# Performance work log

Hardware: AMD Instinct MI355X
Metric: run time of the kernel (lower is better)

The kernel has to match this reference:

```python
import jax, jax.numpy as jnp
import numpy as np

N_NODES = 10000
N_EDGES = 200000
CHANNELS = 128
# lm -> l map for spherical harmonics up to l=3 (1+3+5+7 = 16 components)
L_OF_LM = jnp.array([0, 1, 1, 1, 2, 2, 2, 2, 2, 3, 3, 3, 3, 3, 3, 3], dtype=jnp.int32)


def setup_inputs() -> dict:
    key = jax.random.key(0)
    k1, k2, k3, k4, k5 = jax.random.split(key, 5)
    node_feats = jax.random.normal(k1, (N_NODES, CHANNELS), dtype=jnp.float32)
    edge_attrs = jax.random.normal(k2, (N_EDGES, 16), dtype=jnp.float32)
    tp_weights = jax.random.normal(k3, (N_EDGES, 4, CHANNELS), dtype=jnp.float32)
    sender_list = jax.random.randint(k4, (N_EDGES,), 0, N_NODES, dtype=jnp.int64)
    receiver_list = jnp.sort(jax.random.randint(k5, (N_EDGES,), 0, N_NODES, dtype=jnp.int64))
    return {
        "node_feats": node_feats,
        "edge_attrs": edge_attrs,
        "tp_weights": tp_weights,
        "sender_list": sender_list,
        "receiver_list": receiver_list,
    }


def reference(node_feats, edge_attrs, tp_weights, sender_list, receiver_list):
    # Gather sender features: [E, C]
    sender_feats = node_feats[sender_list]
    # Broadcast per-l weights to the 16 lm components: [E, 16, C]
    w_lm = tp_weights[:, L_OF_LM, :]
    # Per-edge invariant tensor product message: [E, 16, C]
    messages = sender_feats[:, None, :] * edge_attrs[:, :, None] * w_lm
    # Scatter-add to receivers: [N, 16, C]
    out = jax.ops.segment_sum(messages, receiver_list, num_segments=N_NODES)
    return out
```

## Files before the change

### kernel.cpp

```cpp
#include <hip/hip_runtime.h>


#define N_NODES  10000
#define N_EDGES  200000
#define CHANNELS 128

__global__ __launch_bounds__(128) void imp_tp_kernel(
    const float* __restrict__ node_feats,
    const float* __restrict__ edge_attrs,
    const float* __restrict__ tp_weights,
    const int*   __restrict__ sender_list,
    const int*   __restrict__ receiver_list,
    float* __restrict__ out)
{
    const int n = blockIdx.x;
    const int c = threadIdx.x;

    int lo = 0, hi = N_EDGES;
    while (lo < hi) { int mid = (lo + hi) >> 1; if (receiver_list[mid] < n)     lo = mid + 1; else hi = mid; }
    const int seg_start = lo;
    hi = N_EDGES;
    while (lo < hi) { int mid = (lo + hi) >> 1; if (receiver_list[mid] < n + 1) lo = mid + 1; else hi = mid; }
    const int seg_end = lo;

    float acc[16];
    #pragma unroll
    for (int i = 0; i < 16; ++i) acc[i] = 0.0f;

    const float4* __restrict__ ea4 = (const float4*)edge_attrs;

    for (int e = seg_start; e < seg_end; ++e) {
        const int s = sender_list[e];
        const float sf = node_feats[(size_t)s * CHANNELS + c];

        const float* __restrict__ w = tp_weights + (size_t)e * 4 * CHANNELS + c;
        const float w0 = w[0 * CHANNELS];
        const float w1 = w[1 * CHANNELS];
        const float w2 = w[2 * CHANNELS];
        const float w3 = w[3 * CHANNELS];

        const float4 a0 = ea4[(size_t)e * 4 + 0];
        const float4 a1 = ea4[(size_t)e * 4 + 1];
        const float4 a2 = ea4[(size_t)e * 4 + 2];
        const float4 a3 = ea4[(size_t)e * 4 + 3];

        const float p0 = sf * w0;
        const float p1 = sf * w1;
        const float p2 = sf * w2;
        const float p3 = sf * w3;

        acc[0]  = fmaf(p0, a0.x, acc[0]);
        acc[1]  = fmaf(p1, a0.y, acc[1]);
        acc[2]  = fmaf(p1, a0.z, acc[2]);
        acc[3]  = fmaf(p1, a0.w, acc[3]);
        acc[4]  = fmaf(p2, a1.x, acc[4]);
        acc[5]  = fmaf(p2, a1.y, acc[5]);
        acc[6]  = fmaf(p2, a1.z, acc[6]);
        acc[7]  = fmaf(p2, a1.w, acc[7]);
        acc[8]  = fmaf(p2, a2.x, acc[8]);
        acc[9]  = fmaf(p3, a2.y, acc[9]);
        acc[10] = fmaf(p3, a2.z, acc[10]);
        acc[11] = fmaf(p3, a2.w, acc[11]);
        acc[12] = fmaf(p3, a3.x, acc[12]);
        acc[13] = fmaf(p3, a3.y, acc[13]);
        acc[14] = fmaf(p3, a3.z, acc[14]);
        acc[15] = fmaf(p3, a3.w, acc[15]);
    }

    float* __restrict__ o = out + (size_t)n * 16 * CHANNELS + c;
    #pragma unroll
    for (int lm = 0; lm < 16; ++lm) o[lm * CHANNELS] = acc[lm];
}

extern "C" void kernel_launch(void* const* d_in, const int* in_sizes, int n_in,
                              void* d_out, int out_size, void* d_ws, size_t ws_size,
                              hipStream_t stream) {
    const float* node_feats    = (const float*)d_in[0];
    const float* edge_attrs    = (const float*)d_in[1];
    const float* tp_weights    = (const float*)d_in[2];
    const int*   sender_list   = (const int*)d_in[3];
    const int*   receiver_list = (const int*)d_in[4];
    float* out = (float*)d_out;

    imp_tp_kernel<<<N_NODES, CHANNELS, 0, stream>>>(
        node_feats, edge_attrs, tp_weights, sender_list, receiver_list, out);
}
```

Measured before the change: 589.0 us.

## Precompute CSR row pointers and process one node per wavefront with float2 channels

```diff
diff --git a/kernel.cpp b/kernel.cpp
--- a/kernel.cpp
+++ b/kernel.cpp
@@ -3,73 +3,92 @@
 
 #define N_NODES  10000
 #define N_EDGES  200000
-#define CHANNELS 128
 
-__global__ __launch_bounds__(128) void imp_tp_kernel(
+__global__ __launch_bounds__(256) void bounds_kernel(
+    const int* __restrict__ recv, int* __restrict__ row_ptr)
+{
+    const int i = blockIdx.x * 256 + threadIdx.x;
+    if (i > N_NODES) return;
+    int lo = 0, hi = N_EDGES;
+    while (lo < hi) { int mid = (lo + hi) >> 1; if (recv[mid] < i) lo = mid + 1; else hi = mid; }
+    row_ptr[i] = lo;
+}
+
+struct Edge {
+    float2 sf, w0, w1, w2, w3;
+    float4 a0, a1, a2, a3;
+};
+
+#define FMA2(ac, p, s) do { (ac).x = fmaf((p).x, (s), (ac).x); (ac).y = fmaf((p).y, (s), (ac).y); } while (0)
+
+__global__ __launch_bounds__(256) void imp_tp_kernel(
     const float* __restrict__ node_feats,
     const float* __restrict__ edge_attrs,
     const float* __restrict__ tp_weights,
     const int*   __restrict__ sender_list,
-    const int*   __restrict__ receiver_list,
+    const int*   __restrict__ row_ptr,
     float* __restrict__ out)
 {
-    const int n = blockIdx.x;
-    const int c = threadIdx.x;
+    const int lane = threadIdx.x & 63;
+    const int n    = blockIdx.x * 4 + (threadIdx.x >> 6);
+    const int c    = lane * 2;
 
-    int lo = 0, hi = N_EDGES;
-    while (lo < hi) { int mid = (lo + hi) >> 1; if (receiver_list[mid] < n)     lo = mid + 1; else hi = mid; }
-    const int seg_start = lo;
-    hi = N_EDGES;
-    while (lo < hi) { int mid = (lo + hi) >> 1; if (receiver_list[mid] < n + 1) lo = mid + 1; else hi = mid; }
-    const int seg_end = lo;
+    const int lo = __builtin_amdgcn_readfirstlane(row_ptr[n]);
+    const int hi = __builtin_amdgcn_readfirstlane(row_ptr[n + 1]);
 
-    float acc[16];
+    float2 acc[16];
     #pragma unroll
-    for (int i = 0; i < 16; ++i) acc[i] = 0.0f;
+    for (int i = 0; i < 16; ++i) acc[i] = make_float2(0.f, 0.f);
 
-    const float4* __restrict__ ea4 = (const float4*)edge_attrs;
+    auto load_edge = [&](Edge& E, int e) {
+        const int s = __builtin_amdgcn_readfirstlane(sender_list[e]);
+        E.sf = *(const float2*)(node_feats + (size_t)s * 128 + c);
+        const float* wp = tp_weights + (size_t)e * 512 + c;
+        E.w0 = *(const float2*)(wp);
+        E.w1 = *(const float2*)(wp + 128);
+        E.w2 = *(const float2*)(wp + 256);
+        E.w3 = *(const float2*)(wp + 384);
+        const float4* ap = (const float4*)(edge_attrs + (size_t)e * 16);
+        E.a0 = ap[0]; E.a1 = ap[1]; E.a2 = ap[2]; E.a3 = ap[3];
+    };
 
-    for (int e = seg_start; e < seg_end; ++e) {
-        const int s = sender_list[e];
-        const float sf = node_feats[(size_t)s * CHANNELS + c];
+    auto accum_edge = [&](const Edge& E) {
+        float2 p0, p1, p2, p3;
+        p0.x = E.sf.x * E.w0.x; p0.y = E.sf.y * E.w0.y;
+        p1.x = E.sf.x * E.w1.x; p1.y = E.sf.y * E.w1.y;
+        p2.x = E.sf.x * E.w2.x; p2.y = E.sf.y * E.w2.y;
+        p3.x = E.sf.x * E.w3.x; p3.y = E.sf.y * E.w3.y;
+        FMA2(acc[0],  p0, E.a0.x);
+        FMA2(acc[1],  p1, E.a0.y);
+        FMA2(acc[2],  p1, E.a0.z);
+        FMA2(acc[3],  p1, E.a0.w);
+        FMA2(acc[4],  p2, E.a1.x);
+        FMA2(acc[5],  p2, E.a1.y);
+        FMA2(acc[6],  p2, E.a1.z);
+        FMA2(acc[7],  p2, E.a1.w);
+        FMA2(acc[8],  p2, E.a2.x);
+        FMA2(acc[9],  p3, E.a2.y);
+        FMA2(acc[10], p3, E.a2.z);
+        FMA2(acc[11], p3, E.a2.w);
+        FMA2(acc[12], p3, E.a3.x);
+        FMA2(acc[13], p3, E.a3.y);
+        FMA2(acc[14], p3, E.a3.z);
+        FMA2(acc[15], p3, E.a3.w);
+    };
 
-        const float* __restrict__ w = tp_weights + (size_t)e * 4 * CHANNELS + c;
-        const float w0 = w[0 * CHANNELS];
-        const float w1 = w[1 * CHANNELS];
-        const float w2 = w[2 * CHANNELS];
-        const float w3 = w[3 * CHANNELS];
+    Edge A, B;
+    int e = lo;
+    for (; e + 1 < hi; e += 2) {
+        load_edge(A, e);
+        load_edge(B, e + 1);
+        accum_edge(A);
+        accum_edge(B);
+    }
+    if (e < hi) { load_edge(A, e); accum_edge(A); }
 
-        const float4 a0 = ea4[(size_t)e * 4 + 0];
-        const float4 a1 = ea4[(size_t)e * 4 + 1];
-        const float4 a2 = ea4[(size_t)e * 4 + 2];
-        const float4 a3 = ea4[(size_t)e * 4 + 3];
-
-        const float p0 = sf * w0;
-        const float p1 = sf * w1;
-        const float p2 = sf * w2;
-        const float p3 = sf * w3;
-
-        acc[0]  = fmaf(p0, a0.x, acc[0]);
-        acc[1]  = fmaf(p1, a0.y, acc[1]);
-        acc[2]  = fmaf(p1, a0.z, acc[2]);
-        acc[3]  = fmaf(p1, a0.w, acc[3]);
-        acc[4]  = fmaf(p2, a1.x, acc[4]);
-        acc[5]  = fmaf(p2, a1.y, acc[5]);
-        acc[6]  = fmaf(p2, a1.z, acc[6]);
-        acc[7]  = fmaf(p2, a1.w, acc[7]);
-        acc[8]  = fmaf(p2, a2.x, acc[8]);
-        acc[9]  = fmaf(p3, a2.y, acc[9]);
-        acc[10] = fmaf(p3, a2.z, acc[10]);
-        acc[11] = fmaf(p3, a2.w, acc[11]);
-        acc[12] = fmaf(p3, a3.x, acc[12]);
-        acc[13] = fmaf(p3, a3.y, acc[13]);
-        acc[14] = fmaf(p3, a3.z, acc[14]);
-        acc[15] = fmaf(p3, a3.w, acc[15]);
-    }
-
-    float* __restrict__ o = out + (size_t)n * 16 * CHANNELS + c;
+    float* __restrict__ o = out + (size_t)n * 2048 + c;
     #pragma unroll
-    for (int lm = 0; lm < 16; ++lm) o[lm * CHANNELS] = acc[lm];
+    for (int lm = 0; lm < 16; ++lm) *(float2*)(o + lm * 128) = acc[lm];
 }
 
 extern "C" void kernel_launch(void* const* d_in, const int* in_sizes, int n_in,
@@ -80,8 +99,10 @@
     const float* tp_weights    = (const float*)d_in[2];
     const int*   sender_list   = (const int*)d_in[3];
     const int*   receiver_list = (const int*)d_in[4];
-    float* out = (float*)d_out;
+    float* out    = (float*)d_out;
+    int* row_ptr  = (int*)d_ws;
 
-    imp_tp_kernel<<<N_NODES, CHANNELS, 0, stream>>>(
-        node_feats, edge_attrs, tp_weights, sender_list, receiver_list, out);
+    bounds_kernel<<<(N_NODES + 256) / 256, 256, 0, stream>>>(receiver_list, row_ptr);
+    imp_tp_kernel<<<N_NODES / 4, 256, 0, stream>>>(
+        node_feats, edge_attrs, tp_weights, sender_list, row_ptr, out);
 }
```

Result: no change. 585.4 us (-0.6%).
